# Performance work log

Hardware: AMD Instinct MI355X
Metric: run time of the kernel (lower is better)

The kernel has to match this reference:

```python
import jax, jax.numpy as jnp
import numpy as np

INPUT_DIMS = 768
EMBED_DIMS = 768


def setup_inputs() -> dict:
    key = jax.random.key(0)
    k_x, k_w, k_b = jax.random.split(key, 3)
    x = jax.random.normal(k_x, (8, 2048, INPUT_DIMS), dtype=jnp.float32)
    # nn.Linear(input_dims, 3*embed_dims): weight [3E, D], bias [3E]
    bound = 1.0 / np.sqrt(INPUT_DIMS)
    W = jax.random.uniform(k_w, (3 * EMBED_DIMS, INPUT_DIMS), minval=-bound, maxval=bound, dtype=jnp.float32)
    b = jax.random.uniform(k_b, (3 * EMBED_DIMS,), minval=-bound, maxval=bound, dtype=jnp.float32)
    return {"x": x, "W": W, "b": b}


def reference(x, W, b):
    B, L, _ = x.shape
    E = EMBED_DIMS
    scale = E ** (-0.5)
    # fused QKV projection: [B, L, 3E]
    qkv = jnp.einsum('bld,ed->ble', x, W) + b
    qkv = qkv.reshape(B, L, 3, E).transpose(2, 0, 1, 3)  # [3, B, L, E]
    q, k, v = qkv[0], qkv[1], qkv[2]
    scores = jnp.einsum('bqe,bke->bqk', q, k) * scale  # [B, L, L]
    attn = jax.nn.softmax(scores, axis=-1)
    out = jnp.einsum('bqk,bke->bqe', attn, v)  # [B, L, E]
    return out
```

## Files before the change

kernel.cpp:

```cpp
#include <hip/hip_runtime.h>
#include <hip/hip_bf16.h>

typedef __attribute__((ext_vector_type(8))) short bf16x8;
typedef __attribute__((ext_vector_type(4))) float f32x4;
typedef __attribute__((ext_vector_type(8))) unsigned short ushort8;

typedef __attribute__((address_space(1))) void gvoid_as1;
typedef __attribute__((address_space(3))) void lvoid_as3;

__device__ __forceinline__ void gload_lds16(const void* g, void* l) {
  __builtin_amdgcn_global_load_lds((const gvoid_as1*)g, (lvoid_as3*)l, 16, 0, 0);
}

__device__ __forceinline__ unsigned short f2b(float f) {
  __hip_bfloat16 h = __float2bfloat16(f);
  return __builtin_bit_cast(unsigned short, h);
}

__global__ __launch_bounds__(256) void cvt_all(const float* __restrict__ x,
                                               const float* __restrict__ W,
                                               unsigned short* __restrict__ xb,
                                               unsigned short* __restrict__ wb) {
  int i = blockIdx.x * blockDim.x + threadIdx.x;
  const float* src;
  unsigned short* dst;
  int j;
  if (i < 3145728) {
    src = x; dst = xb; j = i;
  } else {
    src = W; dst = wb; j = i - 3145728;
    if (j >= 442368) return;
  }
  float4 v = reinterpret_cast<const float4*>(src)[j];
  ushort4 o;
  o.x = f2b(v.x); o.y = f2b(v.y); o.z = f2b(v.z); o.w = f2b(v.w);
  reinterpret_cast<ushort4*>(dst)[j] = o;
}

template<int EPI>
__global__ __launch_bounds__(256, 4)
void gemm128(const unsigned short* __restrict__ A, int lda, long sA,
             const unsigned short* __restrict__ Bm, int ldb, long sB,
             void* __restrict__ Cv, int ldc, long sC,
             const float* __restrict__ bias, float scale,
             unsigned short* __restrict__ vt,
             float* __restrict__ Lpart, const float* __restrict__ Linv, int K) {
  __shared__ unsigned short lsAB[16384];
  char* const lds = (char*)lsAB;
  const int tid = threadIdx.x;
  const int lane = tid & 63;
  const int wv = tid >> 6;
  const int wr = (wv >> 1) * 64;
  const int wc = (wv & 1) * 64;
  const int lr = lane & 15;
  const int lkb = (lane >> 4) * 16;
  const int swz = (lane & 7) << 4;

  const int gx = gridDim.x;
  const int gxy = gx * gridDim.y;
  const int nwg = gxy * gridDim.z;
  const int orig = (blockIdx.z * gridDim.y + blockIdx.y) * gx + blockIdx.x;
  const int xcd = orig & 7, idx = orig >> 3;
  const int q8 = nwg >> 3, r8 = nwg & 7;
  const int wg = (xcd < r8 ? xcd * (q8 + 1) : r8 * (q8 + 1) + (xcd - r8) * q8) + idx;
  const int bz = wg / gxy;
  const int rem = wg - bz * gxy;
  const int brow = (rem / gx) * 128;
  const int bcol = (rem % gx) * 128;

  const unsigned short* Ab = A + (size_t)bz * sA;
  const unsigned short* Bb = Bm + (size_t)bz * sB;

  f32x4 acc[4][4];
#pragma unroll
  for (int m = 0; m < 4; m++)
#pragma unroll
    for (int n = 0; n < 4; n++) acc[m][n] = (f32x4){0.f, 0.f, 0.f, 0.f};

  for (int kk = 0; kk < K; kk += 64) {
#pragma unroll
    for (int j = 0; j < 4; j++) {
      const int s = tid + j * 256;
      const int r = s >> 3;
      const int c = ((s & 7) ^ (r & 7)) * 8;
      gload_lds16(Ab + (size_t)(brow + r) * lda + kk + c, lds + s * 16);
      gload_lds16(Bb + (size_t)(bcol + r) * ldb + kk + c, lds + 16384 + s * 16);
    }
    __syncthreads();
    bf16x8 af[4][2], bfr[4][2];
#pragma unroll
    for (int m = 0; m < 4; m++)
#pragma unroll
      for (int ks = 0; ks < 2; ks++)
        af[m][ks] = *(const bf16x8*)(lds + (wr + m * 16 + lr) * 128 +
                                     ((ks * 64 + lkb) ^ swz));
#pragma unroll
    for (int n = 0; n < 4; n++)
#pragma unroll
      for (int ks = 0; ks < 2; ks++)
        bfr[n][ks] = *(const bf16x8*)(lds + 16384 + (wc + n * 16 + lr) * 128 +
                                      ((ks * 64 + lkb) ^ swz));
#pragma unroll
    for (int m = 0; m < 4; m++)
#pragma unroll
      for (int n = 0; n < 4; n++) {
        acc[m][n] = __builtin_amdgcn_mfma_f32_16x16x32_bf16(af[m][0], bfr[n][0], acc[m][n], 0, 0, 0);
        acc[m][n] = __builtin_amdgcn_mfma_f32_16x16x32_bf16(af[m][1], bfr[n][1], acc[m][n], 0, 0, 0);
      }
    __syncthreads();
  }

  if (EPI == 2) {
    float* C = (float*)Cv + (size_t)bz * sC;
    const int r0e = brow + wr + (lane >> 4) * 4;
    const float* Lb = Linv + (size_t)bz * 2048;
    float li[4][4];
#pragma unroll
    for (int m = 0; m < 4; m++)
#pragma unroll
      for (int j = 0; j < 4; j++) li[m][j] = Lb[r0e + m * 16 + j];
    const int myh = wr >> 6;
#pragma unroll
    for (int h = 0; h < 2; ++h) {
      if (myh == h) {
#pragma unroll
        for (int m = 0; m < 4; m++)
#pragma unroll
          for (int n = 0; n < 4; n++)
#pragma unroll
            for (int j = 0; j < 4; j++) {
              const int R = (wr & 63) + m * 16 + (lane >> 4) * 4 + j;
              const int Cc = wc + n * 16 + lr;
              *(float*)(lds + R * 512 + ((Cc * 4) ^ ((R & 7) << 4))) =
                  acc[m][n][j] * li[m][j];
            }
      }
      __syncthreads();
      float* Ch = C + (size_t)(brow + h * 64) * ldc + bcol;
#pragma unroll
      for (int i = 0; i < 8; i++) {
        const int id = tid + i * 256;
        const int row = id >> 5, sl = id & 31;
        float4 vv = *(const float4*)(lds + row * 512 +
                                     ((sl * 16) ^ ((row & 7) << 4)));
        *(float4*)(Ch + (size_t)row * ldc + sl * 4) = vv;
      }
      __syncthreads();
    }
  } else {
    const bool isV = (EPI == 0) && (bcol >= 1536);
    const bool isQ = (EPI == 0) && (bcol < 768);
    float bv[4];
    if (EPI == 0) {
#pragma unroll
      for (int n = 0; n < 4; n++) bv[n] = bias[bcol + wc + n * 16 + lr];
    }
    float rs[4][4];
    if (EPI == 1) {
#pragma unroll
      for (int m = 0; m < 4; m++)
#pragma unroll
        for (int j = 0; j < 4; j++) rs[m][j] = 0.f;
    }
#pragma unroll
    for (int m = 0; m < 4; m++)
#pragma unroll
      for (int n = 0; n < 4; n++)
#pragma unroll
        for (int j = 0; j < 4; j++) {
          float v = acc[m][n][j];
          if (EPI == 0) {
            v += bv[n];
            if (isQ) v *= scale;
          }
          if (EPI == 1) {
            v = exp2f(v * 1.4426950408889634f);
            rs[m][j] += v;
          }
          const int R = wr + (lane >> 4) * 4 + m * 16 + j;
          const int Cc = wc + n * 16 + lr;
          const int row_ = isV ? Cc : R;
          const int col_ = isV ? R : Cc;
          *(unsigned short*)(lds + row_ * 256 +
                             ((col_ * 2) ^ ((row_ & 15) << 4))) = f2b(v);
        }
    if (EPI == 1) {
#pragma unroll
      for (int m = 0; m < 4; m++)
#pragma unroll
        for (int j = 0; j < 4; j++) {
          float s = rs[m][j];
          s += __shfl_xor(s, 1);
          s += __shfl_xor(s, 2);
          s += __shfl_xor(s, 4);
          s += __shfl_xor(s, 8);
          rs[m][j] = s;
        }
      if (lr == 0) {
        float* Lp = Lpart + ((size_t)bz * 2048 + brow + wr +
                             (lane >> 4) * 4) * 32 + (bcol >> 7) * 2 + (wv & 1);
#pragma unroll
        for (int m = 0; m < 4; m++)
#pragma unroll
          for (int j = 0; j < 4; j++) Lp[(size_t)(m * 16 + j) * 32] = rs[m][j];
      }
    }
    __syncthreads();
    if (isV) {
      const int b = brow >> 11;
      const int l0 = brow & 2047;
      const int e0 = bcol - 1536;
      unsigned short* dst = vt + ((size_t)b * 768 + e0) * 2048 + l0;
#pragma unroll
      for (int i = 0; i < 8; i++) {
        const int id = tid + i * 256;
        const int row = id >> 4, sl = id & 15;
        ushort8 vv = *(const ushort8*)(lds + row * 256 +
                                       ((sl * 16) ^ ((row & 15) << 4)));
        *(ushort8*)(dst + (size_t)row * 2048 + sl * 8) = vv;
      }
    } else {
      unsigned short* C = (unsigned short*)Cv + (size_t)bz * sC +
                          (size_t)brow * ldc + bcol;
#pragma unroll
      for (int i = 0; i < 8; i++) {
        const int id = tid + i * 256;
        const int row = id >> 4, sl = id & 15;
        ushort8 vv = *(const ushort8*)(lds + row * 256 +
                                       ((sl * 16) ^ ((row & 15) << 4)));
        *(ushort8*)(C + (size_t)row * ldc + sl * 8) = vv;
      }
    }
  }
}

__global__ __launch_bounds__(256) void sum_l(const float* __restrict__ Lpart,
                                             float* __restrict__ Linv, int nrows) {
  int r = blockIdx.x * blockDim.x + threadIdx.x;
  if (r >= nrows) return;
  const float4* p = (const float4*)(Lpart + (size_t)r * 32);
  float s = 0.f;
#pragma unroll
  for (int i = 0; i < 8; i++) {
    float4 v = p[i];
    s += (v.x + v.y) + (v.z + v.w);
  }
  Linv[r] = 1.0f / s;
}

extern "C" void kernel_launch(void* const* d_in, const int* in_sizes, int n_in,
                              void* d_out, int out_size, void* d_ws, size_t ws_size,
                              hipStream_t stream) {
  const float* x = (const float*)d_in[0];
  const float* W = (const float*)d_in[1];
  const float* bias = (const float*)d_in[2];
  float* out = (float*)d_out;
  char* ws = (char*)d_ws;

  unsigned short* xb = (unsigned short*)(ws);
  unsigned short* wb = (unsigned short*)(ws + 25165824);
  unsigned short* qkv = (unsigned short*)(ws + 28704768);
  unsigned short* vt = (unsigned short*)(ws + 104202240);
  unsigned short* S = (unsigned short*)(ws + 129368064);
  float* Lpart = (float*)(ws);
  float* Linv = (float*)(ws + 2097152);
  const float scale = 0.03608439182435161f;

  cvt_all<<<14016, 256, 0, stream>>>(x, W, xb, wb);
  gemm128<0><<<dim3(18, 128, 1), 256, 0, stream>>>(
      xb, 768, 0, wb, 768, 0, qkv, 2304, 0, bias, scale, vt,
      nullptr, nullptr, 768);

  bool batched = ws_size >= (129368064UL + 67108864UL);
  if (batched) {
    gemm128<1><<<dim3(16, 16, 8), 256, 0, stream>>>(
        qkv, 2304, 2048L * 2304, qkv + 768, 2304, 2048L * 2304,
        S, 2048, 2048L * 2048, nullptr, 1.f, nullptr, Lpart, nullptr, 768);
    sum_l<<<64, 256, 0, stream>>>(Lpart, Linv, 16384);
    gemm128<2><<<dim3(6, 16, 8), 256, 0, stream>>>(
        S, 2048, 2048L * 2048, vt, 2048, 768L * 2048,
        out, 768, 2048L * 768, nullptr, 1.f, nullptr, nullptr, Linv, 2048);
  } else {
    for (int b = 0; b < 8; b++) {
      const unsigned short* qb = qkv + (size_t)b * 2048 * 2304;
      gemm128<1><<<dim3(16, 16, 1), 256, 0, stream>>>(
          qb, 2304, 0, qb + 768, 2304, 0, S, 2048, 0, nullptr, 1.f, nullptr,
          Lpart, nullptr, 768);
      sum_l<<<8, 256, 0, stream>>>(Lpart, Linv, 2048);
      gemm128<2><<<dim3(6, 16, 1), 256, 0, stream>>>(
          S, 2048, 0, vt + (size_t)b * 768 * 2048, 2048, 0,
          out + (size_t)b * 2048 * 768, 768, 0, nullptr, 1.f, nullptr,
          nullptr, Linv, 2048);
    }
  }
}
```

Before: 200.8 us.

## Use 256x128 tiles with 512-thread blocks for QKV and score GEMMs

Adds a gemmBig kernel with 8 waves per block computing a 256x128 output tile, used for the QKV projection and the QK^T score GEMM. The larger tile halves the number of blocks and reuses each B tile across twice as many rows, cutting global/L2 traffic per FLOP. The PV GEMM keeps the 128x128 path as a separate gemmPV kernel. In exchange, LDS use grows to 48KB per block and the epilogue is staged in two halves, which may lower occupancy.

```diff
diff --git a/kernel.cpp b/kernel.cpp
--- a/kernel.cpp
+++ b/kernel.cpp
@@ -38,13 +38,180 @@
 }
 
 template<int EPI>
-__global__ __launch_bounds__(256, 4)
-void gemm128(const unsigned short* __restrict__ A, int lda, long sA,
+__global__ __launch_bounds__(512, 4)
+void gemmBig(const unsigned short* __restrict__ A, int lda, long sA,
              const unsigned short* __restrict__ Bm, int ldb, long sB,
              void* __restrict__ Cv, int ldc, long sC,
              const float* __restrict__ bias, float scale,
              unsigned short* __restrict__ vt,
-             float* __restrict__ Lpart, const float* __restrict__ Linv, int K) {
+             float* __restrict__ Lpart, int K) {
+  __shared__ char lds[49152];
+  const int tid = threadIdx.x;
+  const int lane = tid & 63;
+  const int wv = tid >> 6;
+  const int wrow = (wv >> 1) * 64;
+  const int wcol = (wv & 1) * 64;
+  const int lr = lane & 15;
+  const int lkb = (lane >> 4) * 16;
+  const int swz = (lane & 7) << 4;
+
+  const int gx = gridDim.x;
+  const int gxy = gx * gridDim.y;
+  const int nwg = gxy * gridDim.z;
+  const int orig = (blockIdx.z * gridDim.y + blockIdx.y) * gx + blockIdx.x;
+  const int xcd = orig & 7, idx = orig >> 3;
+  const int q8 = nwg >> 3, r8 = nwg & 7;
+  const int wg = (xcd < r8 ? xcd * (q8 + 1) : r8 * (q8 + 1) + (xcd - r8) * q8) + idx;
+  const int bz = wg / gxy;
+  const int rem = wg - bz * gxy;
+  const int brow = (rem / gx) * 256;
+  const int bcol = (rem % gx) * 128;
+
+  const unsigned short* Ab = A + (size_t)bz * sA;
+  const unsigned short* Bb = Bm + (size_t)bz * sB;
+
+  f32x4 acc[4][4];
+#pragma unroll
+  for (int m = 0; m < 4; m++)
+#pragma unroll
+    for (int n = 0; n < 4; n++) acc[m][n] = (f32x4){0.f, 0.f, 0.f, 0.f};
+
+  for (int kk = 0; kk < K; kk += 64) {
+#pragma unroll
+    for (int j = 0; j < 4; j++) {
+      const int s = tid + j * 512;
+      const int r = s >> 3;
+      const int c = ((s & 7) ^ (r & 7)) * 8;
+      gload_lds16(Ab + (size_t)(brow + r) * lda + kk + c, lds + s * 16);
+    }
+#pragma unroll
+    for (int j = 0; j < 2; j++) {
+      const int s = tid + j * 512;
+      const int r = s >> 3;
+      const int c = ((s & 7) ^ (r & 7)) * 8;
+      gload_lds16(Bb + (size_t)(bcol + r) * ldb + kk + c, lds + 32768 + s * 16);
+    }
+    __syncthreads();
+    bf16x8 af[4][2], bfr[4][2];
+#pragma unroll
+    for (int m = 0; m < 4; m++)
+#pragma unroll
+      for (int ks = 0; ks < 2; ks++)
+        af[m][ks] = *(const bf16x8*)(lds + (wrow + m * 16 + lr) * 128 +
+                                     ((ks * 64 + lkb) ^ swz));
+#pragma unroll
+    for (int n = 0; n < 4; n++)
+#pragma unroll
+      for (int ks = 0; ks < 2; ks++)
+        bfr[n][ks] = *(const bf16x8*)(lds + 32768 + (wcol + n * 16 + lr) * 128 +
+                                      ((ks * 64 + lkb) ^ swz));
+#pragma unroll
+    for (int m = 0; m < 4; m++)
+#pragma unroll
+      for (int n = 0; n < 4; n++) {
+        acc[m][n] = __builtin_amdgcn_mfma_f32_16x16x32_bf16(af[m][0], bfr[n][0], acc[m][n], 0, 0, 0);
+        acc[m][n] = __builtin_amdgcn_mfma_f32_16x16x32_bf16(af[m][1], bfr[n][1], acc[m][n], 0, 0, 0);
+      }
+    __syncthreads();
+  }
+
+  const bool isV = (EPI == 0) && (bcol >= 1536);
+  const bool isQ = (EPI == 0) && (bcol < 768);
+  float bv[4];
+  if (EPI == 0) {
+#pragma unroll
+    for (int n = 0; n < 4; n++) bv[n] = bias[bcol + wcol + n * 16 + lr];
+  }
+  float rs[4][4];
+  if (EPI == 1) {
+#pragma unroll
+    for (int m = 0; m < 4; m++)
+#pragma unroll
+      for (int j = 0; j < 4; j++) rs[m][j] = 0.f;
+  }
+  const int myh = wrow >> 7;
+#pragma unroll
+  for (int h = 0; h < 2; ++h) {
+    if (myh == h) {
+#pragma unroll
+      for (int m = 0; m < 4; m++)
+#pragma unroll
+        for (int n = 0; n < 4; n++)
+#pragma unroll
+          for (int j = 0; j < 4; j++) {
+            float v = acc[m][n][j];
+            if (EPI == 0) {
+              v += bv[n];
+              if (isQ) v *= scale;
+            }
+            if (EPI == 1) {
+              v = exp2f(v * 1.4426950408889634f);
+              rs[m][j] += v;
+            }
+            const int Rl = (wrow & 64) + m * 16 + (lane >> 4) * 4 + j;
+            const int Cc = wcol + n * 16 + lr;
+            const int row_ = isV ? Cc : Rl;
+            const int col_ = isV ? Rl : Cc;
+            *(unsigned short*)(lds + row_ * 256 +
+                               ((col_ * 2) ^ ((row_ & 15) << 4))) = f2b(v);
+          }
+    }
+    __syncthreads();
+    if (isV) {
+      const int b = brow >> 11;
+      const int l0 = (brow & 2047) + h * 128;
+      const int e0 = bcol - 1536;
+      unsigned short* dst = vt + ((size_t)b * 768 + e0) * 2048 + l0;
+#pragma unroll
+      for (int i = 0; i < 4; i++) {
+        const int id = tid + i * 512;
+        const int row = id >> 4, sl = id & 15;
+        ushort8 vv = *(const ushort8*)(lds + row * 256 +
+                                       ((sl * 16) ^ ((row & 15) << 4)));
+        *(ushort8*)(dst + (size_t)row * 2048 + sl * 8) = vv;
+      }
+    } else {
+      unsigned short* C = (unsigned short*)Cv + (size_t)bz * sC +
+                          (size_t)(brow + h * 128) * ldc + bcol;
+#pragma unroll
+      for (int i = 0; i < 4; i++) {
+        const int id = tid + i * 512;
+        const int row = id >> 4, sl = id & 15;
+        ushort8 vv = *(const ushort8*)(lds + row * 256 +
+                                       ((sl * 16) ^ ((row & 15) << 4)));
+        *(ushort8*)(C + (size_t)row * ldc + sl * 8) = vv;
+      }
+    }
+    __syncthreads();
+  }
+  if (EPI == 1) {
+#pragma unroll
+    for (int m = 0; m < 4; m++)
+#pragma unroll
+      for (int j = 0; j < 4; j++) {
+        float s = rs[m][j];
+        s += __shfl_xor(s, 1);
+        s += __shfl_xor(s, 2);
+        s += __shfl_xor(s, 4);
+        s += __shfl_xor(s, 8);
+        rs[m][j] = s;
+      }
+    if (lr == 0) {
+      float* Lp = Lpart + ((size_t)bz * 2048 + brow + wrow +
+                           (lane >> 4) * 4) * 32 + (bcol >> 7) * 2 + (wv & 1);
+#pragma unroll
+      for (int m = 0; m < 4; m++)
+#pragma unroll
+        for (int j = 0; j < 4; j++) Lp[(size_t)(m * 16 + j) * 32] = rs[m][j];
+    }
+  }
+}
+
+__global__ __launch_bounds__(256, 4)
+void gemmPV(const unsigned short* __restrict__ A, int lda, long sA,
+            const unsigned short* __restrict__ Bm, int ldb, long sB,
+            float* __restrict__ Cv, int ldc, long sC,
+            const float* __restrict__ Linv, int K) {
   __shared__ unsigned short lsAB[16384];
   char* const lds = (char*)lsAB;
   const int tid = threadIdx.x;
@@ -110,127 +277,41 @@
     __syncthreads();
   }
 
-  if (EPI == 2) {
-    float* C = (float*)Cv + (size_t)bz * sC;
-    const int r0e = brow + wr + (lane >> 4) * 4;
-    const float* Lb = Linv + (size_t)bz * 2048;
-    float li[4][4];
-#pragma unroll
-    for (int m = 0; m < 4; m++)
-#pragma unroll
-      for (int j = 0; j < 4; j++) li[m][j] = Lb[r0e + m * 16 + j];
-    const int myh = wr >> 6;
-#pragma unroll
-    for (int h = 0; h < 2; ++h) {
-      if (myh == h) {
-#pragma unroll
-        for (int m = 0; m < 4; m++)
-#pragma unroll
-          for (int n = 0; n < 4; n++)
-#pragma unroll
-            for (int j = 0; j < 4; j++) {
-              const int R = (wr & 63) + m * 16 + (lane >> 4) * 4 + j;
-              const int Cc = wc + n * 16 + lr;
-              *(float*)(lds + R * 512 + ((Cc * 4) ^ ((R & 7) << 4))) =
-                  acc[m][n][j] * li[m][j];
-            }
-      }
-      __syncthreads();
-      float* Ch = C + (size_t)(brow + h * 64) * ldc + bcol;
-#pragma unroll
-      for (int i = 0; i < 8; i++) {
-        const int id = tid + i * 256;
-        const int row = id >> 5, sl = id & 31;
-        float4 vv = *(const float4*)(lds + row * 512 +
-                                     ((sl * 16) ^ ((row & 7) << 4)));
-        *(float4*)(Ch + (size_t)row * ldc + sl * 4) = vv;
-      }
-      __syncthreads();
-    }
-  } else {
-    const bool isV = (EPI == 0) && (bcol >= 1536);
-    const bool isQ = (EPI == 0) && (bcol < 768);
-    float bv[4];
-    if (EPI == 0) {
-#pragma unroll
-      for (int n = 0; n < 4; n++) bv[n] = bias[bcol + wc + n * 16 + lr];
-    }
-    float rs[4][4];
-    if (EPI == 1) {
+  float* C = Cv + (size_t)bz * sC;
+  const int r0e = brow + wr + (lane >> 4) * 4;
+  const float* Lb = Linv + (size_t)bz * 2048;
+  float li[4][4];
+#pragma unroll
+  for (int m = 0; m < 4; m++)
+#pragma unroll
+    for (int j = 0; j < 4; j++) li[m][j] = Lb[r0e + m * 16 + j];
+  const int myh = wr >> 6;
+#pragma unroll
+  for (int h = 0; h < 2; ++h) {
+    if (myh == h) {
 #pragma unroll
       for (int m = 0; m < 4; m++)
 #pragma unroll
-        for (int j = 0; j < 4; j++) rs[m][j] = 0.f;
-    }
-#pragma unroll
-    for (int m = 0; m < 4; m++)
-#pragma unroll
-      for (int n = 0; n < 4; n++)
-#pragma unroll
-        for (int j = 0; j < 4; j++) {
-          float v = acc[m][n][j];
-          if (EPI == 0) {
-            v += bv[n];
-            if (isQ) v *= scale;
+        for (int n = 0; n < 4; n++)
+#pragma unroll
+          for (int j = 0; j < 4; j++) {
+            const int R = (wr & 63) + m * 16 + (lane >> 4) * 4 + j;
+            const int Cc = wc + n * 16 + lr;
+            *(float*)(lds + R * 512 + ((Cc * 4) ^ ((R & 7) << 4))) =
+                acc[m][n][j] * li[m][j];
           }
-          if (EPI == 1) {
-            v = exp2f(v * 1.4426950408889634f);
-            rs[m][j] += v;
-          }
-          const int R = wr + (lane >> 4) * 4 + m * 16 + j;
-          const int Cc = wc + n * 16 + lr;
-          const int row_ = isV ? Cc : R;
-          const int col_ = isV ? R : Cc;
-          *(unsigned short*)(lds + row_ * 256 +
-                             ((col_ * 2) ^ ((row_ & 15) << 4))) = f2b(v);
-        }
-    if (EPI == 1) {
-#pragma unroll
-      for (int m = 0; m < 4; m++)
-#pragma unroll
-        for (int j = 0; j < 4; j++) {
-          float s = rs[m][j];
-          s += __shfl_xor(s, 1);
-          s += __shfl_xor(s, 2);
-          s += __shfl_xor(s, 4);
-          s += __shfl_xor(s, 8);
-          rs[m][j] = s;
-        }
-      if (lr == 0) {
-        float* Lp = Lpart + ((size_t)bz * 2048 + brow + wr +
-                             (lane >> 4) * 4) * 32 + (bcol >> 7) * 2 + (wv & 1);
-#pragma unroll
-        for (int m = 0; m < 4; m++)
-#pragma unroll
-          for (int j = 0; j < 4; j++) Lp[(size_t)(m * 16 + j) * 32] = rs[m][j];
-      }
-    }
-    __syncthreads();
-    if (isV) {
-      const int b = brow >> 11;
-      const int l0 = brow & 2047;
-      const int e0 = bcol - 1536;
-      unsigned short* dst = vt + ((size_t)b * 768 + e0) * 2048 + l0;
-#pragma unroll
-      for (int i = 0; i < 8; i++) {
-        const int id = tid + i * 256;
-        const int row = id >> 4, sl = id & 15;
-        ushort8 vv = *(const ushort8*)(lds + row * 256 +
-                                       ((sl * 16) ^ ((row & 15) << 4)));
-        *(ushort8*)(dst + (size_t)row * 2048 + sl * 8) = vv;
-      }
-    } else {
-      unsigned short* C = (unsigned short*)Cv + (size_t)bz * sC +
-                          (size_t)brow * ldc + bcol;
-#pragma unroll
-      for (int i = 0; i < 8; i++) {
-        const int id = tid + i * 256;
-        const int row = id >> 4, sl = id & 15;
-        ushort8 vv = *(const ushort8*)(lds + row * 256 +
-                                       ((sl * 16) ^ ((row & 15) << 4)));
-        *(ushort8*)(C + (size_t)row * ldc + sl * 8) = vv;
-      }
-    }
+    }
+    __syncthreads();
+    float* Ch = C + (size_t)(brow + h * 64) * ldc + bcol;
+#pragma unroll
+    for (int i = 0; i < 8; i++) {
+      const int id = tid + i * 256;
+      const int row = id >> 5, sl = id & 31;
+      float4 vv = *(const float4*)(lds + row * 512 +
+                                   ((sl * 16) ^ ((row & 7) << 4)));
+      *(float4*)(Ch + (size_t)row * ldc + sl * 4) = vv;
+    }
+    __syncthreads();
   }
 }
 
@@ -267,30 +348,28 @@
   const float scale = 0.03608439182435161f;
 
   cvt_all<<<14016, 256, 0, stream>>>(x, W, xb, wb);
-  gemm128<0><<<dim3(18, 128, 1), 256, 0, stream>>>(
-      xb, 768, 0, wb, 768, 0, qkv, 2304, 0, bias, scale, vt,
-      nullptr, nullptr, 768);
+  gemmBig<0><<<dim3(18, 64, 1), 512, 0, stream>>>(
+      xb, 768, 0, wb, 768, 0, qkv, 2304, 0, bias, scale, vt, nullptr, 768);
 
   bool batched = ws_size >= (129368064UL + 67108864UL);
   if (batched) {
-    gemm128<1><<<dim3(16, 16, 8), 256, 0, stream>>>(
+    gemmBig<1><<<dim3(16, 8, 8), 512, 0, stream>>>(
         qkv, 2304, 2048L * 2304, qkv + 768, 2304, 2048L * 2304,
-        S, 2048, 2048L * 2048, nullptr, 1.f, nullptr, Lpart, nullptr, 768);
+        S, 2048, 2048L * 2048, nullptr, 1.f, nullptr, Lpart, 768);
     sum_l<<<64, 256, 0, stream>>>(Lpart, Linv, 16384);
-    gemm128<2><<<dim3(6, 16, 8), 256, 0, stream>>>(
+    gemmPV<<<dim3(6, 16, 8), 256, 0, stream>>>(
         S, 2048, 2048L * 2048, vt, 2048, 768L * 2048,
-        out, 768, 2048L * 768, nullptr, 1.f, nullptr, nullptr, Linv, 2048);
+        out, 768, 2048L * 768, Linv, 2048);
   } else {
     for (int b = 0; b < 8; b++) {
       const unsigned short* qb = qkv + (size_t)b * 2048 * 2304;
-      gemm128<1><<<dim3(16, 16, 1), 256, 0, stream>>>(
+      gemmBig<1><<<dim3(16, 8, 1), 512, 0, stream>>>(
           qb, 2304, 0, qb + 768, 2304, 0, S, 2048, 0, nullptr, 1.f, nullptr,
-          Lpart, nullptr, 768);
+          Lpart, 768);
       sum_l<<<8, 256, 0, stream>>>(Lpart, Linv, 2048);
-      gemm128<2><<<dim3(6, 16, 1), 256, 0, stream>>>(
+      gemmPV<<<dim3(6, 16, 1), 256, 0, stream>>>(
           S, 2048, 0, vt + (size_t)b * 768 * 2048, 2048, 0,
-          out + (size_t)b * 2048 * 768, 768, 0, nullptr, 1.f, nullptr,
-          nullptr, Linv, 2048);
-    }
-  }
-}
+          out + (size_t)b * 2048 * 768, 768, 0, Linv, 2048);
+    }
+  }
+}
```

Measured after the change: 206.1 us. +2.6%, slower.
